# Kernel tuning notes

Measured on AMD Instinct MI355X. Metric: run time of the kernel, lower is better.

## Reference

```python
import jax, jax.numpy as jnp
import numpy as np

B, T, C, H, L, V = 4, 1024, 1024, 16, 6, 32000
D = C // H
STD = 0.02


def setup_inputs() -> dict:
    key = jax.random.key(0)
    ks = jax.random.split(key, 12)
    return {
        "idx": jax.random.randint(ks[0], (B, T), 0, V),
        "tok_emb": jax.random.normal(ks[1], (V, C), jnp.float32) * STD,
        "pos_emb": jax.random.normal(ks[2], (T, C), jnp.float32) * STD,
        "qkv_w": jax.random.normal(ks[3], (L, C, 3 * C), jnp.float32) * STD,
        "attn_out_w": jax.random.normal(ks[4], (L, C, C), jnp.float32) * STD,
        "attn_out_b": jnp.zeros((L, C), jnp.float32),
        "fc1_w": jax.random.normal(ks[5], (L, C, 4 * C), jnp.float32) * STD,
        "fc1_b": jnp.zeros((L, 4 * C), jnp.float32),
        "fc2_w": jax.random.normal(ks[6], (L, 4 * C, C), jnp.float32) * STD,
        "fc2_b": jnp.zeros((L, C), jnp.float32),
        "ln1_w": jnp.ones((L, C), jnp.float32),
        "ln1_b": jnp.zeros((L, C), jnp.float32),
        "ln2_w": jnp.ones((L, C), jnp.float32),
        "ln2_b": jnp.zeros((L, C), jnp.float32),
        "lnf_w": jnp.ones((C,), jnp.float32),
        "lnf_b": jnp.zeros((C,), jnp.float32),
        "head_w": jax.random.normal(ks[7], (C, V), jnp.float32) * STD,
    }


def layernorm(x, w, b, eps=1e-5):
    mu = jnp.mean(x, axis=-1, keepdims=True)
    var = jnp.var(x, axis=-1, keepdims=True)
    return (x - mu) * jax.lax.rsqrt(var + eps) * w + b


def attention(x, qkv_w, out_w, out_b, causal_mask):
    # x: (B,T,C)
    qkv = jnp.einsum("btc,cf->btf", x, qkv_w)  # (B,T,3C)
    q, k, v = jnp.split(qkv, 3, axis=-1)
    q = q.reshape(B, T, H, D).transpose(0, 2, 1, 3)  # (B,H,T,D)
    k = k.reshape(B, T, H, D).transpose(0, 2, 1, 3)
    v = v.reshape(B, T, H, D).transpose(0, 2, 1, 3)
    scores = jnp.einsum("bhqd,bhkd->bhqk", q, k) / np.sqrt(D).astype(np.float32)
    scores = jnp.where(causal_mask, scores, -jnp.inf)
    w = jax.nn.softmax(scores, axis=-1)
    out = jnp.einsum("bhqk,bhkd->bhqd", w, v)  # (B,H,T,D)
    out = out.transpose(0, 2, 1, 3).reshape(B, T, C)
    return jnp.einsum("btc,cd->btd", out, out_w) + out_b


def reference(idx, tok_emb, pos_emb, qkv_w, attn_out_w, attn_out_b,
              fc1_w, fc1_b, fc2_w, fc2_b, ln1_w, ln1_b, ln2_w, ln2_b,
              lnf_w, lnf_b, head_w):
    causal_mask = jnp.tril(jnp.ones((T, T), dtype=bool))[None, None]  # (1,1,T,T)
    x = tok_emb[idx] + pos_emb[jnp.arange(T)][None]  # (B,T,C)
    for l in range(L):
        h = layernorm(x, ln1_w[l], ln1_b[l])
        x = x + attention(h, qkv_w[l], attn_out_w[l], attn_out_b[l], causal_mask)
        h = layernorm(x, ln2_w[l], ln2_b[l])
        h = jax.nn.relu(jnp.einsum("btc,cf->btf", h, fc1_w[l]) + fc1_b[l])
        x = x + jnp.einsum("btf,fc->btc", h, fc2_w[l]) + fc2_b[l]
    x = layernorm(x, lnf_w, lnf_b)
    logits = jnp.einsum("btc,cv->btv", x, head_w)  # (B,T,V)
    return logits
```

## Files before the change

kernel.cpp:

```cpp
#include <hip/hip_runtime.h>
#include <cstdint>
#include <cstddef>

typedef __bf16 bf16_t;
typedef __bf16 bf16x8 __attribute__((ext_vector_type(8)));
typedef float f32x4 __attribute__((ext_vector_type(4)));
typedef int i32x4 __attribute__((ext_vector_type(4)));

#define B_ 4
#define T_ 1024
#define C_ 1024
#define H_ 16
#define L_ 6
#define V_ 32000
#define M_ (B_ * T_)

__global__ __launch_bounds__(256) void k_embed(const int* __restrict__ idx,
                                               const float* __restrict__ tok,
                                               const float* __restrict__ pos,
                                               float* __restrict__ x) {
  int row = blockIdx.x;
  int t = row & (T_ - 1);
  int id = idx[row];
  int c = threadIdx.x * 4;
  f32x4 a = *(const f32x4*)(tok + (size_t)id * C_ + c);
  f32x4 p = *(const f32x4*)(pos + (size_t)t * C_ + c);
  *(f32x4*)(x + (size_t)row * C_ + c) = a + p;
}

__global__ __launch_bounds__(256) void k_ln(const float* __restrict__ x,
                                            const float* __restrict__ w,
                                            const float* __restrict__ b,
                                            bf16_t* __restrict__ out) {
  __shared__ float red[8];
  int row = blockIdx.x;
  int tid = threadIdx.x;
  const float* xr = x + (size_t)row * C_;
  f32x4 v = *(const f32x4*)(xr + tid * 4);
  float s = v[0] + v[1] + v[2] + v[3];
  float q = v[0] * v[0] + v[1] * v[1] + v[2] * v[2] + v[3] * v[3];
#pragma unroll
  for (int off = 32; off; off >>= 1) {
    s += __shfl_xor(s, off);
    q += __shfl_xor(q, off);
  }
  int wid = tid >> 6;
  if ((tid & 63) == 0) { red[wid * 2] = s; red[wid * 2 + 1] = q; }
  __syncthreads();
  s = red[0] + red[2] + red[4] + red[6];
  q = red[1] + red[3] + red[5] + red[7];
  float mu = s * (1.f / C_);
  float var = q * (1.f / C_) - mu * mu;
  float rstd = rsqrtf(var + 1e-5f);
  f32x4 wv = *(const f32x4*)(w + tid * 4);
  f32x4 bv = *(const f32x4*)(b + tid * 4);
  bf16_t* o = out + (size_t)row * C_ + tid * 4;
#pragma unroll
  for (int j = 0; j < 4; j++) o[j] = (bf16_t)((v[j] - mu) * rstd * wv[j] + bv[j]);
}

__global__ __launch_bounds__(256) void k_transpose_bf16(const float* __restrict__ in,
                                                        bf16_t* __restrict__ out,
                                                        int K, int N) {
  __shared__ float tile[32][33];
  int n0 = blockIdx.x * 32, k0 = blockIdx.y * 32;
  int tid = threadIdx.x;
  int cr = tid >> 5, cc = tid & 31;
#pragma unroll
  for (int it = 0; it < 4; it++) {
    int r = it * 8 + cr;
    tile[r][cc] = in[(size_t)(k0 + r) * N + n0 + cc];
  }
  __syncthreads();
#pragma unroll
  for (int it = 0; it < 4; it++) {
    int r = it * 8 + cr;
    out[(size_t)(n0 + r) * K + k0 + cc] = (bf16_t)tile[cc][r];
  }
}

__global__ __launch_bounds__(256) void k_reshape_qk(const bf16_t* __restrict__ qkv,
                                                    bf16_t* __restrict__ qh,
                                                    bf16_t* __restrict__ kh) {
  int g = blockIdx.x * 256 + threadIdx.x;
  int d = g & 63;
  int t = (g >> 6) & (T_ - 1);
  int h = (g >> 16) & (H_ - 1);
  int b = g >> 20;
  size_t src = ((size_t)(b * T_ + t)) * (3 * C_) + h * 64 + d;
  qh[g] = (bf16_t)((float)qkv[src] * 0.125f);
  kh[g] = qkv[src + C_];
}

__global__ __launch_bounds__(256) void k_vtrans(const bf16_t* __restrict__ qkv,
                                                bf16_t* __restrict__ vT) {
  __shared__ bf16_t tile[64][65];
  int bh = blockIdx.x;
  int t0 = blockIdx.y * 64;
  int tid = threadIdx.x;
  int c = tid & 63, rr = tid >> 6;
  int b = bh >> 4, h = bh & (H_ - 1);
  const bf16_t* src = qkv + ((size_t)(b * T_ + t0)) * (3 * C_) + 2 * C_ + h * 64;
#pragma unroll
  for (int it = 0; it < 16; it++) {
    int r = it * 4 + rr;
    tile[r][c] = src[(size_t)r * (3 * C_) + c];
  }
  __syncthreads();
  bf16_t* dst = vT + (size_t)bh * 64 * T_ + t0;
#pragma unroll
  for (int it = 0; it < 16; it++) {
    int dr = it * 4 + rr;
    dst[(size_t)dr * T_ + c] = tile[c][dr];
  }
}

__global__ __launch_bounds__(256) void k_attn(const bf16_t* __restrict__ qh,
                                              const bf16_t* __restrict__ kh,
                                              const bf16_t* __restrict__ vT,
                                              bf16_t* __restrict__ outb) {
  __shared__ bf16_t p_lds[4][16 * 32];
  int tid = threadIdx.x, lane = tid & 63, wid = tid >> 6;
  int bh = blockIdx.x;
  int b = bh >> 4, h = bh & (H_ - 1);
  int qbase = blockIdx.y * 64 + wid * 16;
  const bf16_t* qp = qh + ((size_t)bh * T_ + qbase) * 64;
  const bf16_t* kp = kh + (size_t)bh * T_ * 64;
  const bf16_t* vp = vT + (size_t)bh * 64 * T_;
  int r = lane & 15, g = lane >> 4;

  bf16x8 qf0 = *(const bf16x8*)(qp + r * 64 + g * 8);
  bf16x8 qf1 = *(const bf16x8*)(qp + r * 64 + 32 + g * 8);

  f32x4 o[4];
  float m[4], l[4];
#pragma unroll
  for (int j = 0; j < 4; j++) { m[j] = -1e30f; l[j] = 0.f; o[j] = (f32x4){0.f, 0.f, 0.f, 0.f}; }

  int kv_end = qbase + 16;
  for (int jb = 0; jb < kv_end; jb += 32) {
    f32x4 s0 = (f32x4){0.f, 0.f, 0.f, 0.f};
    f32x4 s1 = (f32x4){0.f, 0.f, 0.f, 0.f};
    const bf16_t* kb0 = kp + (size_t)(jb + r) * 64 + g * 8;
    const bf16_t* kb1 = kb0 + 16 * 64;
    s0 = __builtin_amdgcn_mfma_f32_16x16x32_bf16(qf0, *(const bf16x8*)(kb0), s0, 0, 0, 0);
    s0 = __builtin_amdgcn_mfma_f32_16x16x32_bf16(qf1, *(const bf16x8*)(kb0 + 32), s0, 0, 0, 0);
    s1 = __builtin_amdgcn_mfma_f32_16x16x32_bf16(qf0, *(const bf16x8*)(kb1), s1, 0, 0, 0);
    s1 = __builtin_amdgcn_mfma_f32_16x16x32_bf16(qf1, *(const bf16x8*)(kb1 + 32), s1, 0, 0, 0);

    float p0[4], p1[4], fac[4];
#pragma unroll
    for (int j = 0; j < 4; j++) {
      int rowg = qbase + g * 4 + j;
      float v0 = s0[j], v1 = s1[j];
      if (jb + r > rowg) v0 = -1e30f;
      if (jb + 16 + r > rowg) v1 = -1e30f;
      float t = fmaxf(v0, v1);
      t = fmaxf(t, __shfl_xor(t, 1));
      t = fmaxf(t, __shfl_xor(t, 2));
      t = fmaxf(t, __shfl_xor(t, 4));
      t = fmaxf(t, __shfl_xor(t, 8));
      float nm = fmaxf(m[j], t);
      p0[j] = __expf(v0 - nm);
      p1[j] = __expf(v1 - nm);
      float f = __expf(m[j] - nm);
      float ts = p0[j] + p1[j];
      ts += __shfl_xor(ts, 1);
      ts += __shfl_xor(ts, 2);
      ts += __shfl_xor(ts, 4);
      ts += __shfl_xor(ts, 8);
      l[j] = l[j] * f + ts;
      m[j] = nm;
      fac[j] = f;
    }
    f32x4 fv = (f32x4){fac[0], fac[1], fac[2], fac[3]};
#pragma unroll
    for (int d = 0; d < 4; d++) o[d] *= fv;

    bf16_t* pl = p_lds[wid];
#pragma unroll
    for (int j = 0; j < 4; j++) {
      pl[(g * 4 + j) * 32 + r] = (bf16_t)p0[j];
      pl[(g * 4 + j) * 32 + 16 + r] = (bf16_t)p1[j];
    }
    bf16x8 pa = *(const bf16x8*)(pl + r * 32 + g * 8);
#pragma unroll
    for (int d = 0; d < 4; d++) {
      const bf16_t* vf = vp + (size_t)(d * 16 + r) * T_ + jb + g * 8;
      o[d] = __builtin_amdgcn_mfma_f32_16x16x32_bf16(pa, *(const bf16x8*)(vf), o[d], 0, 0, 0);
    }
  }

#pragma unroll
  for (int d = 0; d < 4; d++) {
#pragma unroll
    for (int j = 0; j < 4; j++) {
      float val = o[d][j] / l[j];
      outb[((size_t)(b * T_ + qbase + g * 4 + j)) * C_ + h * 64 + d * 16 + r] = (bf16_t)val;
    }
  }
}

__device__ __forceinline__ void gld_lds16(const bf16_t* g, bf16_t* l) {
  __builtin_amdgcn_global_load_lds((const __attribute__((address_space(1))) void*)g,
                                   (__attribute__((address_space(3))) void*)l, 16, 0, 0);
}
__device__ __forceinline__ bf16x8 lds_rd128(uint32_t addr) {
  i32x4 d;
  asm volatile("ds_read_b128 %0, %1" : "=v"(d) : "v"(addr));
  return __builtin_bit_cast(bf16x8, d);
}
#define BAR_() __builtin_amdgcn_s_barrier()
#define SCHED0_() __builtin_amdgcn_sched_barrier(0)
#define WLG0_() do { asm volatile("s_waitcnt lgkmcnt(0)" ::: "memory"); SCHED0_(); } while (0)

template <int OUTBF, int HASB, int HASRELU, int HASRES>
__global__ __launch_bounds__(256) void k_gemm(const bf16_t* __restrict__ A,
                                              const bf16_t* __restrict__ Bt,
                                              const float* __restrict__ bias,
                                              const float* resid,
                                              void* Cout, int M, int N, int K) {
  __shared__ bf16_t As[2][128 * 32];
  __shared__ bf16_t Bs[2][128 * 32];
  int tid = threadIdx.x;
  int lane = tid & 63, wid = tid >> 6;
  size_t rowBase = (size_t)blockIdx.y * 128;
  size_t colBase = (size_t)blockIdx.x * 128;

  const bf16_t* gA = A + (rowBase + (tid >> 2)) * (size_t)K + (tid & 3) * 8;
  const bf16_t* gB = Bt + (colBase + (tid >> 2)) * (size_t)K + (tid & 3) * 8;
  const size_t gStep64 = (size_t)64 * K;

  f32x4 acc[4][4];
#pragma unroll
  for (int i = 0; i < 4; i++)
#pragma unroll
    for (int j = 0; j < 4; j++) acc[i][j] = (f32x4){0.f, 0.f, 0.f, 0.f};

  int NK = K >> 5;
  {
    bf16_t* la = &As[0][0] + wid * 512;
    bf16_t* lb = &Bs[0][0] + wid * 512;
    gld_lds16(gA, la);            gld_lds16(gA + gStep64, la + 2048);
    gld_lds16(gB, lb);            gld_lds16(gB + gStep64, lb + 2048);
  }

  int wr = (wid >> 1) * 64, wc = (wid & 1) * 64;
  int r15 = lane & 15, g4 = lane >> 4;

  for (int kt = 0; kt < NK; kt++) {
    int buf = kt & 1;
    __syncthreads();
    if (kt + 1 < NK) {
      const bf16_t* ga = gA + (size_t)(kt + 1) * 32;
      const bf16_t* gb = gB + (size_t)(kt + 1) * 32;
      bf16_t* la = &As[buf ^ 1][0] + wid * 512;
      bf16_t* lb = &Bs[buf ^ 1][0] + wid * 512;
      gld_lds16(ga, la);          gld_lds16(ga + gStep64, la + 2048);
      gld_lds16(gb, lb);          gld_lds16(gb + gStep64, lb + 2048);
    }
    const bf16_t* as = &As[buf][0] + (wr + r15) * 32 + g4 * 8;
    const bf16_t* bs = &Bs[buf][0] + (wc + r15) * 32 + g4 * 8;
    bf16x8 af[4], bfr[4];
#pragma unroll
    for (int i = 0; i < 4; i++) af[i] = *(const bf16x8*)(as + i * 16 * 32);
#pragma unroll
    for (int i = 0; i < 4; i++) bfr[i] = *(const bf16x8*)(bs + i * 16 * 32);
#pragma unroll
    for (int i = 0; i < 4; i++)
#pragma unroll
      for (int j = 0; j < 4; j++)
        acc[i][j] = __builtin_amdgcn_mfma_f32_16x16x32_bf16(af[i], bfr[j], acc[i][j], 0, 0, 0);
  }

#pragma unroll
  for (int i = 0; i < 4; i++) {
    size_t row0 = rowBase + wr + i * 16 + g4 * 4;
#pragma unroll
    for (int j = 0; j < 4; j++) {
      size_t col = colBase + wc + j * 16 + r15;
      float bi = HASB ? bias[col] : 0.f;
#pragma unroll
      for (int q = 0; q < 4; q++) {
        size_t row = row0 + q;
        float v = acc[i][j][q] + bi;
        if (HASRELU) v = fmaxf(v, 0.f);
        if (HASRES) v += resid[row * (size_t)N + col];
        if (OUTBF)
          ((bf16_t*)Cout)[row * (size_t)N + col] = (bf16_t)v;
        else
          ((float*)Cout)[row * (size_t)N + col] = v;
      }
    }
  }
}

#define STAGE_(q, tk, bufv)                                                           \
  do {                                                                                \
    const bf16_t* _ga = A + (size_t)(rowBase + (q)*64 + srow) * (size_t)K +           \
                        (size_t)(tk)*64 + scol;                                       \
    const bf16_t* _gb = Bt + (size_t)(colBase + (q)*64 + srow) * (size_t)K +          \
                        (size_t)(tk)*64 + scol;                                       \
    gld_lds16(_ga, AsF + (bufv)*16384 + (q)*4096 + w * 512);                          \
    gld_lds16(_gb, BsF + (bufv)*16384 + (q)*4096 + w * 512);                          \
  } while (0)

#define LDA_(mh, bufv)                                                                \
  do {                                                                                \
    uint32_t _ab = aRd + (uint32_t)(bufv)*32768u + (mh)*8192u;                        \
    _Pragma("unroll") for (int _m = 0; _m < 4; _m++)                                  \
        _Pragma("unroll") for (int _k = 0; _k < 2; _k++)                              \
            af[_m][_k] = lds_rd128(_ab + _m * 2048 + (_k ? offK1 : offK0));           \
  } while (0)

#define LDB_(nh, bufv)                                                                \
  do {                                                                                \
    uint32_t _bb = bRd + (uint32_t)(bufv)*32768u + (nh)*4096u;                        \
    _Pragma("unroll") for (int _n = 0; _n < 2; _n++)                                  \
        _Pragma("unroll") for (int _k = 0; _k < 2; _k++)                              \
            bfr[_n][_k] = lds_rd128(_bb + _n * 2048 + (_k ? offK1 : offK0));          \
  } while (0)

#define MFQ_(mh, nh)                                                                  \
  do {                                                                                \
    __builtin_amdgcn_s_setprio(1);                                                    \
    _Pragma("unroll") for (int _m = 0; _m < 4; _m++)                                  \
        _Pragma("unroll") for (int _n = 0; _n < 2; _n++)                              \
            _Pragma("unroll") for (int _k = 0; _k < 2; _k++)                          \
                acc[(mh)*4 + _m][(nh)*2 + _n] = __builtin_amdgcn_mfma_f32_16x16x32_bf16( \
                    af[_m][_k], bfr[_n][_k], acc[(mh)*4 + _m][(nh)*2 + _n], 0, 0, 0); \
    __builtin_amdgcn_s_setprio(0);                                                    \
  } while (0)

template <int OUTBF, int HASB, int HASRELU, int HASRES>
__global__ __launch_bounds__(512, 2) void k_gemm256(const bf16_t* __restrict__ A,
                                                    const bf16_t* __restrict__ Bt,
                                                    const float* __restrict__ bias,
                                                    const float* resid,
                                                    void* Cout, int M, int N, int K) {
  __shared__ bf16_t As[2][256][64];
  __shared__ bf16_t Bs[2][256][64];
  bf16_t* AsF = &As[0][0][0];
  bf16_t* BsF = &Bs[0][0][0];
  const uint32_t asb = (uint32_t)(uintptr_t)AsF;
  const uint32_t bsb = (uint32_t)(uintptr_t)BsF;

  int tid = threadIdx.x, lane = tid & 63, w = tid >> 6;
  int wr = w >> 2, wc = w & 3;
  int r15 = lane & 15, g4 = lane >> 4;

  int nwg = (int)gridDim.x;
  int bid = (int)blockIdx.x;
  int xcd = bid & 7, loc = bid >> 3;
  int q8 = nwg >> 3, r8 = nwg & 7;
  int swz = (xcd < r8) ? xcd * (q8 + 1) + loc : r8 * (q8 + 1) + (xcd - r8) * q8 + loc;
  int nY = M >> 8;
  int by = swz % nY, bx = swz / nY;
  int rowBase = by * 256, colBase = bx * 256;

  int srow = w * 8 + (lane >> 3);
  int scol = ((lane & 7) ^ (lane >> 3)) * 8;

  uint32_t xm = (uint32_t)((r15 & 7) << 4);
  uint32_t offK0 = ((uint32_t)(g4 * 16)) ^ xm;
  uint32_t offK1 = ((uint32_t)(g4 * 16 + 64)) ^ xm;
  uint32_t aRd = asb + (uint32_t)((wr * 128 + r15) * 128);
  uint32_t bRd = bsb + (uint32_t)((wc * 64 + r15) * 128);

  f32x4 acc[8][4];
#pragma unroll
  for (int i = 0; i < 8; i++)
#pragma unroll
    for (int j = 0; j < 4; j++) acc[i][j] = (f32x4){0.f, 0.f, 0.f, 0.f};

  bf16x8 af[4][2], bfr[2][2];

#pragma unroll
  for (int q = 0; q < 4; q++) STAGE_(q, 0, 0);

  int NT = K >> 6;
  for (int kt = 0; kt < NT; ++kt) {
    int buf = kt & 1;
    bool pf = (kt + 1 < NT);
    if (pf) {
#pragma unroll
      for (int q = 0; q < 4; q++) STAGE_(q, kt + 1, buf ^ 1);
      asm volatile("s_waitcnt vmcnt(8)" ::: "memory");
    } else {
      asm volatile("s_waitcnt vmcnt(0)" ::: "memory");
    }
    BAR_();
    SCHED0_();
    LDA_(0, buf);
    LDB_(0, buf);
    WLG0_();
    MFQ_(0, 0);
    BAR_();
    LDB_(1, buf);
    BAR_();
    WLG0_();
    MFQ_(0, 1);
    BAR_();
    LDA_(1, buf);
    BAR_();
    WLG0_();
    MFQ_(1, 1);
    BAR_();
    LDB_(0, buf);
    BAR_();
    WLG0_();
    MFQ_(1, 0);
    BAR_();
  }

#pragma unroll
  for (int m = 0; m < 8; m++) {
    size_t row0 = (size_t)rowBase + wr * 128 + m * 16 + g4 * 4;
#pragma unroll
    for (int n = 0; n < 4; n++) {
      size_t col = (size_t)colBase + wc * 64 + n * 16 + r15;
      float bi = HASB ? bias[col] : 0.f;
#pragma unroll
      for (int qq = 0; qq < 4; qq++) {
        size_t row = row0 + qq;
        float v = acc[m][n][qq] + bi;
        if (HASRELU) v = fmaxf(v, 0.f);
        if (HASRES) v += resid[row * (size_t)N + col];
        if (OUTBF)
          ((bf16_t*)Cout)[row * (size_t)N + col] = (bf16_t)v;
        else
          ((float*)Cout)[row * (size_t)N + col] = v;
      }
    }
  }
}

extern "C" void kernel_launch(void* const* d_in, const int* in_sizes, int n_in,
                              void* d_out, int out_size, void* d_ws, size_t ws_size,
                              hipStream_t stream) {
  (void)in_sizes; (void)n_in; (void)out_size; (void)ws_size;
  const int* idx = (const int*)d_in[0];
  const float* tok_emb = (const float*)d_in[1];
  const float* pos_emb = (const float*)d_in[2];
  const float* qkv_w = (const float*)d_in[3];
  const float* attn_out_w = (const float*)d_in[4];
  const float* attn_out_b = (const float*)d_in[5];
  const float* fc1_w = (const float*)d_in[6];
  const float* fc1_b = (const float*)d_in[7];
  const float* fc2_w = (const float*)d_in[8];
  const float* fc2_b = (const float*)d_in[9];
  const float* ln1_w = (const float*)d_in[10];
  const float* ln1_b = (const float*)d_in[11];
  const float* ln2_w = (const float*)d_in[12];
  const float* ln2_b = (const float*)d_in[13];
  const float* lnf_w = (const float*)d_in[14];
  const float* lnf_b = (const float*)d_in[15];
  const float* head_w = (const float*)d_in[16];
  float* out = (float*)d_out;

  char* wsp = (char*)d_ws;
  auto alloc = [&](size_t bytes) {
    char* p = wsp;
    wsp += (bytes + 255) & ~(size_t)255;
    return p;
  };
  float* x      = (float*)alloc((size_t)M_ * C_ * 4);
  bf16_t* hbuf  = (bf16_t*)alloc((size_t)M_ * C_ * 2);
  bf16_t* qkvb  = (bf16_t*)alloc((size_t)M_ * 3 * C_ * 2);
  bf16_t* qhb   = (bf16_t*)alloc((size_t)M_ * C_ * 2);
  bf16_t* khb   = (bf16_t*)alloc((size_t)M_ * C_ * 2);
  bf16_t* vTb   = (bf16_t*)alloc((size_t)M_ * C_ * 2);
  bf16_t* attnb = (bf16_t*)alloc((size_t)M_ * C_ * 2);
  bf16_t* midb  = (bf16_t*)alloc((size_t)M_ * 4 * C_ * 2);
  bf16_t* qkvwT = (bf16_t*)alloc((size_t)3 * C_ * C_ * 2);
  bf16_t* owT   = (bf16_t*)alloc((size_t)C_ * C_ * 2);
  bf16_t* fc1wT = (bf16_t*)alloc((size_t)4 * C_ * C_ * 2);
  bf16_t* fc2wT = (bf16_t*)alloc((size_t)4 * C_ * C_ * 2);
  bf16_t* headwT= (bf16_t*)alloc((size_t)C_ * V_ * 2);

  k_embed<<<M_, 256, 0, stream>>>(idx, tok_emb, pos_emb, x);
  k_transpose_bf16<<<dim3(V_ / 32, C_ / 32), 256, 0, stream>>>(head_w, headwT, C_, V_);

  for (int l = 0; l < L_; l++) {
    k_transpose_bf16<<<dim3(3 * C_ / 32, C_ / 32), 256, 0, stream>>>(
        qkv_w + (size_t)l * C_ * 3 * C_, qkvwT, C_, 3 * C_);
    k_transpose_bf16<<<dim3(C_ / 32, C_ / 32), 256, 0, stream>>>(
        attn_out_w + (size_t)l * C_ * C_, owT, C_, C_);
    k_transpose_bf16<<<dim3(4 * C_ / 32, C_ / 32), 256, 0, stream>>>(
        fc1_w + (size_t)l * C_ * 4 * C_, fc1wT, C_, 4 * C_);
    k_transpose_bf16<<<dim3(C_ / 32, 4 * C_ / 32), 256, 0, stream>>>(
        fc2_w + (size_t)l * 4 * C_ * C_, fc2wT, 4 * C_, C_);

    k_ln<<<M_, 256, 0, stream>>>(x, ln1_w + l * C_, ln1_b + l * C_, hbuf);
    k_gemm256<1, 0, 0, 0><<<dim3((3 * C_ / 256) * (M_ / 256)), 512, 0, stream>>>(
        hbuf, qkvwT, nullptr, nullptr, qkvb, M_, 3 * C_, C_);
    k_reshape_qk<<<(M_ * C_) / 256, 256, 0, stream>>>(qkvb, qhb, khb);
    k_vtrans<<<dim3(B_ * H_, T_ / 64), 256, 0, stream>>>(qkvb, vTb);
    k_attn<<<dim3(B_ * H_, T_ / 64), 256, 0, stream>>>(qhb, khb, vTb, attnb);
    k_gemm<0, 1, 0, 1><<<dim3(C_ / 128, M_ / 128), 256, 0, stream>>>(
        attnb, owT, attn_out_b + l * C_, x, x, M_, C_, C_);

    k_ln<<<M_, 256, 0, stream>>>(x, ln2_w + l * C_, ln2_b + l * C_, hbuf);
    k_gemm256<1, 1, 1, 0><<<dim3((4 * C_ / 256) * (M_ / 256)), 512, 0, stream>>>(
        hbuf, fc1wT, fc1_b + (size_t)l * 4 * C_, nullptr, midb, M_, 4 * C_, C_);
    k_gemm<0, 1, 0, 1><<<dim3(C_ / 128, M_ / 128), 256, 0, stream>>>(
        midb, fc2wT, fc2_b + l * C_, x, x, M_, C_, 4 * C_);
  }

  k_ln<<<M_, 256, 0, stream>>>(x, lnf_w, lnf_b, hbuf);
  k_gemm256<0, 0, 0, 0><<<dim3((V_ / 256) * (M_ / 256)), 512, 0, stream>>>(
      hbuf, headwT, nullptr, nullptr, out, M_, V_, C_);
}
```

Before: 2.383 ms.

## Restructure 256-tile GEMM loop into register double-buffered K-halves with fewer barriers

The k_gemm256 main loop used to run four quadrant phases per K tile, each with its own LDS read, lgkmcnt(0) wait and barrier. It now splits each 64-wide K tile into two K-halves and double-buffers the fragments in registers (a0/b0, a1/b1). LDS reads for the next half are issued before the MFMAs of the current half, with partial lgkmcnt waits, so far fewer barriers are needed. The cost is more live fragment registers, which could hurt occupancy. The full vmcnt(0) wait is now placed mid-iteration, so global prefetch has less compute to hide behind.

```diff
diff --git a/kernel.cpp b/kernel.cpp
--- a/kernel.cpp
+++ b/kernel.cpp
@@ -212,7 +212,11 @@
 }
 #define BAR_() __builtin_amdgcn_s_barrier()
 #define SCHED0_() __builtin_amdgcn_sched_barrier(0)
-#define WLG0_() do { asm volatile("s_waitcnt lgkmcnt(0)" ::: "memory"); SCHED0_(); } while (0)
+#define WLGN_(n)                                                           \
+  do {                                                                     \
+    asm volatile("s_waitcnt lgkmcnt(" #n ")" ::: "memory");                \
+    SCHED0_();                                                             \
+  } while (0)
 
 template <int OUTBF, int HASB, int HASRELU, int HASRES>
 __global__ __launch_bounds__(256) void k_gemm(const bf16_t* __restrict__ A,
@@ -305,30 +309,24 @@
     gld_lds16(_gb, BsF + (bufv)*16384 + (q)*4096 + w * 512);                          \
   } while (0)
 
-#define LDA_(mh, bufv)                                                                \
+#define RDS_(aset, bset, kk, bufv)                                                    \
   do {                                                                                \
-    uint32_t _ab = aRd + (uint32_t)(bufv)*32768u + (mh)*8192u;                        \
-    _Pragma("unroll") for (int _m = 0; _m < 4; _m++)                                  \
-        _Pragma("unroll") for (int _k = 0; _k < 2; _k++)                              \
-            af[_m][_k] = lds_rd128(_ab + _m * 2048 + (_k ? offK1 : offK0));           \
+    uint32_t _off = (kk) ? offK1 : offK0;                                             \
+    uint32_t _ab = aRd + (uint32_t)(bufv)*32768u + _off;                              \
+    uint32_t _bb = bRd + (uint32_t)(bufv)*32768u + _off;                              \
+    _Pragma("unroll") for (int _m = 0; _m < 8; _m++)                                  \
+        aset[_m] = lds_rd128(_ab + _m * 2048);                                        \
+    _Pragma("unroll") for (int _n = 0; _n < 4; _n++)                                  \
+        bset[_n] = lds_rd128(_bb + _n * 2048);                                        \
   } while (0)
 
-#define LDB_(nh, bufv)                                                                \
-  do {                                                                                \
-    uint32_t _bb = bRd + (uint32_t)(bufv)*32768u + (nh)*4096u;                        \
-    _Pragma("unroll") for (int _n = 0; _n < 2; _n++)                                  \
-        _Pragma("unroll") for (int _k = 0; _k < 2; _k++)                              \
-            bfr[_n][_k] = lds_rd128(_bb + _n * 2048 + (_k ? offK1 : offK0));          \
-  } while (0)
-
-#define MFQ_(mh, nh)                                                                  \
+#define MFH_(aset, bset)                                                              \
   do {                                                                                \
     __builtin_amdgcn_s_setprio(1);                                                    \
-    _Pragma("unroll") for (int _m = 0; _m < 4; _m++)                                  \
-        _Pragma("unroll") for (int _n = 0; _n < 2; _n++)                              \
-            _Pragma("unroll") for (int _k = 0; _k < 2; _k++)                          \
-                acc[(mh)*4 + _m][(nh)*2 + _n] = __builtin_amdgcn_mfma_f32_16x16x32_bf16( \
-                    af[_m][_k], bfr[_n][_k], acc[(mh)*4 + _m][(nh)*2 + _n], 0, 0, 0); \
+    _Pragma("unroll") for (int _m = 0; _m < 8; _m++)                                  \
+        _Pragma("unroll") for (int _n = 0; _n < 4; _n++)                              \
+            acc[_m][_n] = __builtin_amdgcn_mfma_f32_16x16x32_bf16(                    \
+                aset[_m], bset[_n], acc[_m][_n], 0, 0, 0);                            \
     __builtin_amdgcn_s_setprio(0);                                                    \
   } while (0)
 
@@ -373,10 +371,13 @@
 #pragma unroll
     for (int j = 0; j < 4; j++) acc[i][j] = (f32x4){0.f, 0.f, 0.f, 0.f};
 
-  bf16x8 af[4][2], bfr[2][2];
+  bf16x8 a0[8], a1[8], b0[4], b1[4];
 
 #pragma unroll
   for (int q = 0; q < 4; q++) STAGE_(q, 0, 0);
+  asm volatile("s_waitcnt vmcnt(0)" ::: "memory");
+  BAR_();
+  RDS_(a0, b0, 0, 0);
 
   int NT = K >> 6;
   for (int kt = 0; kt < NT; ++kt) {
@@ -385,31 +386,19 @@
     if (pf) {
 #pragma unroll
       for (int q = 0; q < 4; q++) STAGE_(q, kt + 1, buf ^ 1);
-      asm volatile("s_waitcnt vmcnt(8)" ::: "memory");
+    }
+    RDS_(a1, b1, 1, buf);
+    WLGN_(12);
+    MFH_(a0, b0);
+    if (pf) {
+      asm volatile("s_waitcnt vmcnt(0)" ::: "memory");
+      BAR_();
+      RDS_(a0, b0, 0, buf ^ 1);
+      WLGN_(12);
     } else {
-      asm volatile("s_waitcnt vmcnt(0)" ::: "memory");
-    }
-    BAR_();
-    SCHED0_();
-    LDA_(0, buf);
-    LDB_(0, buf);
-    WLG0_();
-    MFQ_(0, 0);
-    BAR_();
-    LDB_(1, buf);
-    BAR_();
-    WLG0_();
-    MFQ_(0, 1);
-    BAR_();
-    LDA_(1, buf);
-    BAR_();
-    WLG0_();
-    MFQ_(1, 1);
-    BAR_();
-    LDB_(0, buf);
-    BAR_();
-    WLG0_();
-    MFQ_(1, 0);
+      WLGN_(0);
+    }
+    MFH_(a1, b1);
     BAR_();
   }
 
```

Result: no change. 2.340 ms (-1.8%).
